# Kernel optimization log

Measured on AMD Instinct MI355X. Metric: run time of the kernel, lower is better.

## Reference

```python
import jax, jax.numpy as jnp
import numpy as np

N = 50000
E = 800000
EP = 200000
IN_C = 128
HID = 128


def setup_inputs() -> dict:
    key = jax.random.key(0)
    ks = jax.random.split(key, 10)
    x = jax.random.normal(ks[0], (N, IN_C), dtype=jnp.float32)
    edge_index = jax.random.randint(ks[1], (2, E), 0, N, dtype=jnp.int64)
    pred_edges = jax.random.randint(ks[2], (2, EP), 0, N, dtype=jnp.int64)
    s_in = 1.0 / np.sqrt(IN_C)
    s_h = 1.0 / np.sqrt(HID)
    W1l = jax.random.normal(ks[3], (IN_C, HID), dtype=jnp.float32) * s_in
    W1r = jax.random.normal(ks[4], (IN_C, HID), dtype=jnp.float32) * s_in
    b1 = jnp.zeros((HID,), dtype=jnp.float32)
    W2l = jax.random.normal(ks[5], (HID, HID), dtype=jnp.float32) * s_h
    W2r = jax.random.normal(ks[6], (HID, HID), dtype=jnp.float32) * s_h
    b2 = jnp.zeros((HID,), dtype=jnp.float32)
    return {"x": x, "W1l": W1l, "b1": b1, "W1r": W1r,
            "W2l": W2l, "b2": b2, "W2r": W2r,
            "edge_index": edge_index, "pred_edges": pred_edges}


def _sage_conv(h, Wl, b, Wr, src, dst, n_nodes):
    # PyG SAGEConv (aggr='mean'): out = lin_l(mean_j x_j) + lin_r(x_i)
    msg = h[src]                                              # (E, D) gather
    agg = jax.ops.segment_sum(msg, dst, num_segments=n_nodes)  # (N, D) scatter-add
    deg = jax.ops.segment_sum(jnp.ones((src.shape[0],), h.dtype), dst,
                              num_segments=n_nodes)
    agg = agg / jnp.maximum(deg, 1.0)[:, None]                # mean (0 for isolated)
    return agg @ Wl + b + h @ Wr


def reference(x, W1l, b1, W1r, W2l, b2, W2r, edge_index, pred_edges):
    n_nodes = x.shape[0]
    src, dst = edge_index[0], edge_index[1]
    h = jax.nn.relu(_sage_conv(x, W1l, b1, W1r, src, dst, n_nodes))
    z = _sage_conv(h, W2l, b2, W2r, src, dst, n_nodes)
    ps, pd = pred_edges[0], pred_edges[1]
    return jnp.sum(z[ps] * z[pd], axis=-1)  # (E_pred,) logits
```

## Files before the change

kernel.cpp:

```cpp
#include <hip/hip_runtime.h>

#define D 128

typedef __attribute__((ext_vector_type(8))) short short8;
typedef __attribute__((ext_vector_type(4))) float f32x4;

__device__ inline unsigned int f2bf_bits(float f) {
    unsigned int u = __float_as_uint(f);
    return (u + 0x7FFFu + ((u >> 16) & 1u)) >> 16;
}

__global__ __launch_bounds__(256) void cast_bf16_kernel(const float* __restrict__ in,
                                                        unsigned short* __restrict__ outb,
                                                        int n4,
                                                        int* __restrict__ chist,
                                                        int* __restrict__ csrpad) {
    if (blockIdx.x == gridDim.x - 1) {
        int t = threadIdx.x;
        chist[t] = 0;
        if (t < 16) csrpad[t] = 0;
        return;
    }
    int i = blockIdx.x * blockDim.x + threadIdx.x;
    if (i >= n4) return;
    f32x4 v = *(const f32x4*)(in + (size_t)i * 4);
    ushort4 o;
    o.x = (unsigned short)f2bf_bits(v.x);
    o.y = (unsigned short)f2bf_bits(v.y);
    o.z = (unsigned short)f2bf_bits(v.z);
    o.w = (unsigned short)f2bf_bits(v.w);
    *(ushort4*)(outb + (size_t)i * 4) = o;
}

__global__ __launch_bounds__(256) void coarse_count_kernel(const int* __restrict__ dst,
                                                           int* __restrict__ chist, int E) {
    __shared__ int h[256];
    h[threadIdx.x] = 0;
    __syncthreads();
    const int stride = gridDim.x * 256;
    for (int e = blockIdx.x * 256 + threadIdx.x; e < E; e += stride)
        atomicAdd(&h[dst[e] >> 8], 1);
    __syncthreads();
    int v = h[threadIdx.x];
    if (v) atomicAdd(&chist[threadIdx.x], v);
}

__global__ __launch_bounds__(256) void scan256_kernel(const int* __restrict__ chist,
                                                      int* __restrict__ cbase,
                                                      int* __restrict__ gcur) {
    __shared__ int wsum[4];
    const int t = threadIdx.x, lane = t & 63, wv = t >> 6;
    int v = chist[t];
    int s = v;
#pragma unroll
    for (int o = 1; o < 64; o <<= 1) {
        int u = __shfl_up(s, o, 64);
        if (lane >= o) s += u;
    }
    if (lane == 63) wsum[wv] = s;
    __syncthreads();
    int add = 0;
    for (int w = 0; w < wv; ++w) add += wsum[w];
    cbase[t + 1] = s + add;
    if (t == 0) cbase[0] = 0;
    gcur[t] = s + add - v;
}

#define CCHUNK 4096
__global__ __launch_bounds__(256) void coarse_scatter_kernel(
    const int* __restrict__ src, const int* __restrict__ dst,
    int* __restrict__ gcur, unsigned int* __restrict__ centries, int E)
{
    __shared__ int h[256];
    __shared__ int base[256];
    __shared__ unsigned int stage[CCHUNK];
    const int t = threadIdx.x;
    const int e0 = blockIdx.x * CCHUNK;
    h[t] = 0;
    __syncthreads();
#pragma unroll
    for (int i = 0; i < 16; ++i) {
        int e = e0 + i * 256 + t;
        unsigned int u = 0xFFFFFFFFu;
        if (e < E) {
            int d = dst[e];
            int s = src[e];
            int b = d >> 8;
            u = ((unsigned)b << 24) | ((unsigned)s << 8) | (unsigned)(d & 255);
            atomicAdd(&h[b], 1);
        }
        stage[i * 256 + t] = u;
    }
    __syncthreads();
    base[t] = atomicAdd(&gcur[t], h[t]);
    __syncthreads();
    h[t] = 0;
    __syncthreads();
#pragma unroll
    for (int i = 0; i < 16; ++i) {
        unsigned int u = stage[i * 256 + t];
        if (u != 0xFFFFFFFFu) {
            int b = u >> 24;
            int r = atomicAdd(&h[b], 1);
            centries[base[b] + r] = u & 0x00FFFFFFu;
        }
    }
}

#define DCAP 8192
__global__ __launch_bounds__(256) void fine_bucket_kernel(
    const unsigned int* __restrict__ centries,
    const int* __restrict__ cbase,
    int* __restrict__ offo, int* __restrict__ csr, int N, int E)
{
    __shared__ int h[256], ex[256], wsum[4];
    __shared__ int stg[DCAP];
    const int t = threadIdx.x, lane = t & 63, wv = t >> 6;
    const int b = blockIdx.x;
    const int s0 = cbase[b];
    const int cnt = cbase[b + 1] - s0;
    h[t] = 0;
    __syncthreads();
    for (int i = t; i < cnt; i += 256)
        atomicAdd(&h[centries[s0 + i] & 255], 1);
    __syncthreads();
    int v = h[t], s = v;
#pragma unroll
    for (int o = 1; o < 64; o <<= 1) {
        int u = __shfl_up(s, o, 64);
        if (lane >= o) s += u;
    }
    if (lane == 63) wsum[wv] = s;
    __syncthreads();
    int add = 0;
    for (int w = 0; w < wv; ++w) add += wsum[w];
    const int exc = s + add - v;
    ex[t] = exc;
    const int dg = b * 256 + t;
    if (dg < N) offo[dg] = s0 + exc;
    if (b == 0 && t == 0) offo[N] = E;
    h[t] = 0;
    __syncthreads();
    if (cnt <= DCAP) {
        for (int i = t; i < cnt; i += 256) {
            unsigned int u = centries[s0 + i];
            int dl = u & 255;
            int r = atomicAdd(&h[dl], 1);
            stg[ex[dl] + r] = (int)(u >> 8);
        }
        __syncthreads();
        for (int i = t; i < cnt; i += 256)
            csr[s0 + i] = stg[i];
    } else {
        for (int i = t; i < cnt; i += 256) {
            unsigned int u = centries[s0 + i];
            int dl = u & 255;
            int r = atomicAdd(&h[dl], 1);
            csr[s0 + ex[dl] + r] = (int)(u >> 8);
        }
    }
}

__global__ __launch_bounds__(256) void wsplit_kernel(const float* __restrict__ W1l,
                                                     const float* __restrict__ W1r,
                                                     const float* __restrict__ W2l,
                                                     const float* __restrict__ W2r,
                                                     unsigned short* __restrict__ h1,
                                                     unsigned short* __restrict__ l1,
                                                     unsigned short* __restrict__ h2,
                                                     unsigned short* __restrict__ l2) {
    int gidx = blockIdx.x * 256 + threadIdx.x;
    int sel = gidx >> 15;
    int idx = gidx & 32767;
    int t = idx >> 12;
    int ks = (idx >> 9) & 7;
    int lane = (idx >> 3) & 63;
    int j = idx & 7;
    int q = lane >> 4, r16 = lane & 15;
    int k = ks * 32 + q * 8 + j;
    int c = t * 16 + r16;
    const float* Wl = sel ? W2l : W1l;
    const float* Wr = sel ? W2r : W1r;
    float v = (k < 128) ? Wl[k * 128 + c] : Wr[(k - 128) * 128 + c];
    unsigned int h = f2bf_bits(v);
    float hf = __uint_as_float(h << 16);
    unsigned int l = f2bf_bits(v - hf);
    (sel ? h2 : h1)[idx] = (unsigned short)h;
    (sel ? l2 : l1)[idx] = (unsigned short)l;
}

__global__ __launch_bounds__(256) void gather_mean_kernel(
    const unsigned short* __restrict__ featbf,
    const int* __restrict__ off,
    const int* __restrict__ csr,
    float* __restrict__ aggp,
    int n_nodes)
{
    const int hw = (blockIdx.x * 256 + threadIdx.x) >> 5;
    const int l5 = threadIdx.x & 31;
    if (hw >= n_nodes) return;
    const unsigned short* fb = featbf + (size_t)l5 * 4;
    const int start = off[hw];
    const int end = off[hw + 1];
    f32x4 acc = {0.f, 0.f, 0.f, 0.f};
    for (int e = start; e < end; e += 16) {
        int4 ia = *(const int4*)(csr + e);
        int4 ib = *(const int4*)(csr + e + 4);
        int4 ic = *(const int4*)(csr + e + 8);
        int4 id = *(const int4*)(csr + e + 12);
        uint2 r[16];
        r[0]  = *(const uint2*)(fb + (size_t)ia.x * D);
        r[1]  = *(const uint2*)(fb + (size_t)ia.y * D);
        r[2]  = *(const uint2*)(fb + (size_t)ia.z * D);
        r[3]  = *(const uint2*)(fb + (size_t)ia.w * D);
        r[4]  = *(const uint2*)(fb + (size_t)ib.x * D);
        r[5]  = *(const uint2*)(fb + (size_t)ib.y * D);
        r[6]  = *(const uint2*)(fb + (size_t)ib.z * D);
        r[7]  = *(const uint2*)(fb + (size_t)ib.w * D);
        r[8]  = *(const uint2*)(fb + (size_t)ic.x * D);
        r[9]  = *(const uint2*)(fb + (size_t)ic.y * D);
        r[10] = *(const uint2*)(fb + (size_t)ic.z * D);
        r[11] = *(const uint2*)(fb + (size_t)ic.w * D);
        r[12] = *(const uint2*)(fb + (size_t)id.x * D);
        r[13] = *(const uint2*)(fb + (size_t)id.y * D);
        r[14] = *(const uint2*)(fb + (size_t)id.z * D);
        r[15] = *(const uint2*)(fb + (size_t)id.w * D);
#pragma unroll
        for (int p = 0; p < 16; ++p) {
            uint2 rv = r[p];
            if (e + p >= end) { rv.x = 0u; rv.y = 0u; }
            acc.x += __uint_as_float(rv.x << 16);
            acc.y += __uint_as_float(rv.x & 0xffff0000u);
            acc.z += __uint_as_float(rv.y << 16);
            acc.w += __uint_as_float(rv.y & 0xffff0000u);
        }
    }
    float dinv = 1.0f / (float)max(end - start, 1);
    acc *= dinv;
    const int tile = hw >> 4, r16 = hw & 15;
    const int ks = l5 >> 3, q = (l5 & 7) >> 1, jb = (l5 & 1) * 4;
    const size_t p = ((size_t)(tile * 4 + ks) * 64 + q * 16 + r16) * 8 + jb;
    *(f32x4*)(aggp + p) = acc;
}

__global__ __launch_bounds__(256) void sage_gemm_kernel(
    const float* __restrict__ aggp,
    const float* __restrict__ selfm,
    const unsigned short* __restrict__ wpk_hi,
    const unsigned short* __restrict__ wpk_lo,
    const float* __restrict__ bias,
    float* __restrict__ outp,
    unsigned short* __restrict__ outbf,
    int ntiles, int self_packed, int do_relu)
{
    const int wv = threadIdx.x >> 6;
    const int lane = threadIdx.x & 63;
    const int tile = blockIdx.x * 4 + wv;
    if (tile >= ntiles) return;
    const int q = lane >> 4, r16 = lane & 15;
    const int n0w = tile * 16;

    f32x4 acc8[8];
#pragma unroll
    for (int t = 0; t < 8; ++t) acc8[t] = (f32x4){0.f, 0.f, 0.f, 0.f};

    const float* ap = aggp + (size_t)tile * 2048 + lane * 8;
    const float* spk = selfm + (size_t)tile * 2048 + lane * 8;
    const float* spr = selfm + (size_t)(n0w + r16) * D + q * 8;

    for (int ks = 0; ks < 8; ++ks) {
        f32x4 a0, a1;
        if (ks < 4) {
            a0 = *(const f32x4*)(ap + ks * 512);
            a1 = *(const f32x4*)(ap + ks * 512 + 4);
        } else if (self_packed) {
            a0 = *(const f32x4*)(spk + (ks - 4) * 512);
            a1 = *(const f32x4*)(spk + (ks - 4) * 512 + 4);
        } else {
            a0 = *(const f32x4*)(spr + (ks - 4) * 32);
            a1 = *(const f32x4*)(spr + (ks - 4) * 32 + 4);
        }
        short8 BH[8], BL[8];
        const unsigned short* bh = wpk_hi + (size_t)ks * 512 + lane * 8;
        const unsigned short* bl = wpk_lo + (size_t)ks * 512 + lane * 8;
#pragma unroll
        for (int t = 0; t < 8; ++t) {
            BH[t] = *(const short8*)(bh + (size_t)t * 4096);
            BL[t] = *(const short8*)(bl + (size_t)t * 4096);
        }
        short8 ahi, alo;
#pragma unroll
        for (int i = 0; i < 8; ++i) {
            float vv = (i < 4) ? a0[i] : a1[i - 4];
            unsigned int h = f2bf_bits(vv);
            float hf = __uint_as_float(h << 16);
            unsigned int l = f2bf_bits(vv - hf);
            ahi[i] = (short)h;
            alo[i] = (short)l;
        }
#pragma unroll
        for (int t = 0; t < 8; ++t) {
            acc8[t] = __builtin_amdgcn_mfma_f32_16x16x32_bf16(ahi, BH[t], acc8[t], 0, 0, 0);
            acc8[t] = __builtin_amdgcn_mfma_f32_16x16x32_bf16(alo, BH[t], acc8[t], 0, 0, 0);
            acc8[t] = __builtin_amdgcn_mfma_f32_16x16x32_bf16(ahi, BL[t], acc8[t], 0, 0, 0);
        }
    }

#pragma unroll
    for (int t = 0; t < 8; ++t) {
        const float bv = bias[t * 16 + r16];
#pragma unroll
        for (int r = 0; r < 4; ++r) {
            float vv = acc8[t][r] + bv;
            if (do_relu) vv = fmaxf(vv, 0.f);
            if (outp) {
                const size_t p = ((size_t)(tile * 4 + (t >> 1)) * 64
                                  + ((t & 1) * 2 + (r16 >> 3)) * 16 + q * 4 + r) * 8
                                 + (r16 & 7);
                outp[p] = vv;
            }
            if (outbf) {
                outbf[(size_t)(n0w + q * 4 + r) * D + t * 16 + r16] =
                    (unsigned short)f2bf_bits(vv);
            }
        }
    }
}

__global__ __launch_bounds__(256) void pred_kernel(const unsigned short* __restrict__ zbf,
                                                   const int* __restrict__ ps,
                                                   const int* __restrict__ pd,
                                                   float* __restrict__ out, int EP) {
    int idx = blockIdx.x * blockDim.x + threadIdx.x;
    int e = idx >> 5;
    if (e >= EP) return;
    int l = idx & 31;
    const unsigned short* fb = zbf + (size_t)l * 4;
    uint2 ra = *(const uint2*)(fb + (size_t)ps[e] * D);
    uint2 rb = *(const uint2*)(fb + (size_t)pd[e] * D);
    float p = __uint_as_float(ra.x << 16)         * __uint_as_float(rb.x << 16)
            + __uint_as_float(ra.x & 0xffff0000u) * __uint_as_float(rb.x & 0xffff0000u)
            + __uint_as_float(ra.y << 16)         * __uint_as_float(rb.y << 16)
            + __uint_as_float(ra.y & 0xffff0000u) * __uint_as_float(rb.y & 0xffff0000u);
#pragma unroll
    for (int off = 16; off > 0; off >>= 1) p += __shfl_xor(p, off, 32);
    if (l == 0) out[e] = p;
}

extern "C" void kernel_launch(void* const* d_in, const int* in_sizes, int n_in,
                              void* d_out, int out_size, void* d_ws, size_t ws_size,
                              hipStream_t stream) {
    const float* x   = (const float*)d_in[0];
    const float* W1l = (const float*)d_in[1];
    const float* b1  = (const float*)d_in[2];
    const float* W1r = (const float*)d_in[3];
    const float* W2l = (const float*)d_in[4];
    const float* b2  = (const float*)d_in[5];
    const float* W2r = (const float*)d_in[6];
    const int* edge_index = (const int*)d_in[7];
    const int* pred_edges = (const int*)d_in[8];
    float* out = (float*)d_out;

    const int N  = in_sizes[0] / D;
    const int E  = in_sizes[7] / 2;
    const int EP = in_sizes[8] / 2;

    const int* src = edge_index;
    const int* dst = edge_index + E;
    const int* ps  = pred_edges;
    const int* pd  = pred_edges + EP;

    int* chist   = (int*)d_ws;
    int* cbase   = chist + 256;
    int* gcur    = cbase + 272;
    int* off     = gcur + 256;
    unsigned int* centries = (unsigned int*)(off + 50016);
    int* csr     = (int*)(centries + E);
    float* aggp  = (float*)(csr + E + 16);
    float* hpk   = aggp + (size_t)N * D;
    unsigned short* w1_hi = (unsigned short*)(hpk + (size_t)N * D);
    unsigned short* w1_lo = w1_hi + 32768;
    unsigned short* w2_hi = w1_lo + 32768;
    unsigned short* w2_lo = w2_hi + 32768;
    unsigned short* fbf   = w2_lo + 32768;

    const int nblk_gather = (N * 32 + 255) / 256;
    const int ntiles = N / 16;
    const int nblk_gemm = (ntiles + 3) / 4;
    const int ncast = (N * D / 4 + 255) / 256;
    const int nbC = (E + CCHUNK - 1) / CCHUNK;
    const int nbD = (N + 255) / 256;

    wsplit_kernel<<<256, 256, 0, stream>>>(W1l, W1r, W2l, W2r, w1_hi, w1_lo, w2_hi, w2_lo);
    cast_bf16_kernel<<<ncast + 1, 256, 0, stream>>>(x, fbf, N * D / 4, chist, csr + E);

    coarse_count_kernel<<<256, 256, 0, stream>>>(dst, chist, E);
    scan256_kernel<<<1, 256, 0, stream>>>(chist, cbase, gcur);
    coarse_scatter_kernel<<<nbC, 256, 0, stream>>>(src, dst, gcur, centries, E);
    fine_bucket_kernel<<<nbD, 256, 0, stream>>>(centries, cbase, off, csr, N, E);

    gather_mean_kernel<<<nblk_gather, 256, 0, stream>>>(fbf, off, csr, aggp, N);
    sage_gemm_kernel<<<nblk_gemm, 256, 0, stream>>>(aggp, x, w1_hi, w1_lo, b1,
                                                    hpk, fbf, ntiles, 0, 1);
    gather_mean_kernel<<<nblk_gather, 256, 0, stream>>>(fbf, off, csr, aggp, N);
    sage_gemm_kernel<<<nblk_gemm, 256, 0, stream>>>(aggp, hpk, w2_hi, w2_lo, b2,
                                                    (float*)nullptr, fbf, ntiles, 1, 0);
    pred_kernel<<<(EP * 32 + 255) / 256, 256, 0, stream>>>(fbf, ps, pd, out, EP);
}
```

Measured before the change: 261.0 us.

## Fuse prep kernels and store GEMM operands pre-split as packed bf16 hi/lo

Merges the weight split, input cast, coarse histogram and pad zeroing into one prep kernel. The histogram now uses per-block partials that the scan kernel reduces, so the global atomics go away. Aggregates and self features are now written as packed bf16 hi/lo pairs instead of fp32, which halves operand bytes and removes the split arithmetic inside the GEMM. Out-of-range gather indices are redirected to a valid row, and bounds checks are dropped on the assumption that N is a multiple of the block sizes. The cost is extra workspace, an extra write of the packed x in prep, and a 256-iteration serial reduction in the scan.

```diff
diff --git a/kernel.cpp b/kernel.cpp
--- a/kernel.cpp
+++ b/kernel.cpp
@@ -9,48 +9,80 @@
     unsigned int u = __float_as_uint(f);
     return (u + 0x7FFFu + ((u >> 16) & 1u)) >> 16;
 }
-
-__global__ __launch_bounds__(256) void cast_bf16_kernel(const float* __restrict__ in,
-                                                        unsigned short* __restrict__ outb,
-                                                        int n4,
-                                                        int* __restrict__ chist,
-                                                        int* __restrict__ csrpad) {
-    if (blockIdx.x == gridDim.x - 1) {
-        int t = threadIdx.x;
-        chist[t] = 0;
+__device__ inline void bfsplit(float v, unsigned short& h, unsigned short& l) {
+    unsigned int hb = f2bf_bits(v);
+    float hf = __uint_as_float(hb << 16);
+    h = (unsigned short)hb;
+    l = (unsigned short)f2bf_bits(v - hf);
+}
+
+__global__ __launch_bounds__(256) void prep_kernel(
+    const float* __restrict__ x,
+    const float* __restrict__ W1l, const float* __restrict__ W1r,
+    const float* __restrict__ W2l, const float* __restrict__ W2r,
+    const int* __restrict__ dst,
+    unsigned short* __restrict__ fbf,
+    unsigned short* __restrict__ xp_hi, unsigned short* __restrict__ xp_lo,
+    unsigned short* __restrict__ w1_hi, unsigned short* __restrict__ w1_lo,
+    unsigned short* __restrict__ w2_hi, unsigned short* __restrict__ w2_lo,
+    int* __restrict__ part, int* __restrict__ csrpad, int E)
+{
+    const int t = threadIdx.x;
+    const int b = blockIdx.x;
+    if (b < 6250) {
+        const int i = b * 256 + t;
+        const int hw = i >> 5, l5 = i & 31;
+        f32x4 v = *(const f32x4*)(x + (size_t)hw * D + l5 * 4);
+        ushort4 hv, lv;
+        bfsplit(v.x, hv.x, lv.x);
+        bfsplit(v.y, hv.y, lv.y);
+        bfsplit(v.z, hv.z, lv.z);
+        bfsplit(v.w, hv.w, lv.w);
+        *(ushort4*)(fbf + (size_t)hw * D + l5 * 4) = hv;
+        const int tile = hw >> 4, r16 = hw & 15;
+        const int ks = l5 >> 3, q = (l5 & 7) >> 1, jb = (l5 & 1) * 4;
+        const size_t p = ((size_t)(tile * 4 + ks) * 64 + q * 16 + r16) * 8 + jb;
+        *(ushort4*)(xp_hi + p) = hv;
+        *(ushort4*)(xp_lo + p) = lv;
+    } else if (b < 6506) {
+        int gidx = (b - 6250) * 256 + t;
+        int sel = gidx >> 15;
+        int idx = gidx & 32767;
+        int tt = idx >> 12;
+        int ks = (idx >> 9) & 7;
+        int lane = (idx >> 3) & 63;
+        int j = idx & 7;
+        int q = lane >> 4, r16 = lane & 15;
+        int k = ks * 32 + q * 8 + j;
+        int c = tt * 16 + r16;
+        const float* Wl = sel ? W2l : W1l;
+        const float* Wr = sel ? W2r : W1r;
+        float v = (k < 128) ? Wl[k * 128 + c] : Wr[(k - 128) * 128 + c];
+        unsigned short h, l;
+        bfsplit(v, h, l);
+        (sel ? w2_hi : w1_hi)[idx] = h;
+        (sel ? w2_lo : w1_lo)[idx] = l;
+    } else if (b < 6762) {
+        __shared__ int h[256];
+        h[t] = 0;
+        __syncthreads();
+        const int b3 = b - 6506;
+        for (int e = b3 * 256 + t; e < E; e += 65536)
+            atomicAdd(&h[dst[e] >> 8], 1);
+        __syncthreads();
+        part[b3 * 256 + t] = h[t];
+    } else {
         if (t < 16) csrpad[t] = 0;
-        return;
-    }
-    int i = blockIdx.x * blockDim.x + threadIdx.x;
-    if (i >= n4) return;
-    f32x4 v = *(const f32x4*)(in + (size_t)i * 4);
-    ushort4 o;
-    o.x = (unsigned short)f2bf_bits(v.x);
-    o.y = (unsigned short)f2bf_bits(v.y);
-    o.z = (unsigned short)f2bf_bits(v.z);
-    o.w = (unsigned short)f2bf_bits(v.w);
-    *(ushort4*)(outb + (size_t)i * 4) = o;
-}
-
-__global__ __launch_bounds__(256) void coarse_count_kernel(const int* __restrict__ dst,
-                                                           int* __restrict__ chist, int E) {
-    __shared__ int h[256];
-    h[threadIdx.x] = 0;
-    __syncthreads();
-    const int stride = gridDim.x * 256;
-    for (int e = blockIdx.x * 256 + threadIdx.x; e < E; e += stride)
-        atomicAdd(&h[dst[e] >> 8], 1);
-    __syncthreads();
-    int v = h[threadIdx.x];
-    if (v) atomicAdd(&chist[threadIdx.x], v);
-}
-
-__global__ __launch_bounds__(256) void scan256_kernel(const int* __restrict__ chist,
+    }
+}
+
+__global__ __launch_bounds__(256) void scan256_kernel(const int* __restrict__ part,
                                                       int* __restrict__ cbase,
                                                       int* __restrict__ gcur) {
     __shared__ int wsum[4];
     const int t = threadIdx.x, lane = t & 63, wv = t >> 6;
-    int v = chist[t];
+    int v = 0;
+    for (int b = 0; b < 256; ++b) v += part[b * 256 + t];
     int s = v;
 #pragma unroll
     for (int o = 1; o < 64; o <<= 1) {
@@ -161,44 +193,15 @@
     }
 }
 
-__global__ __launch_bounds__(256) void wsplit_kernel(const float* __restrict__ W1l,
-                                                     const float* __restrict__ W1r,
-                                                     const float* __restrict__ W2l,
-                                                     const float* __restrict__ W2r,
-                                                     unsigned short* __restrict__ h1,
-                                                     unsigned short* __restrict__ l1,
-                                                     unsigned short* __restrict__ h2,
-                                                     unsigned short* __restrict__ l2) {
-    int gidx = blockIdx.x * 256 + threadIdx.x;
-    int sel = gidx >> 15;
-    int idx = gidx & 32767;
-    int t = idx >> 12;
-    int ks = (idx >> 9) & 7;
-    int lane = (idx >> 3) & 63;
-    int j = idx & 7;
-    int q = lane >> 4, r16 = lane & 15;
-    int k = ks * 32 + q * 8 + j;
-    int c = t * 16 + r16;
-    const float* Wl = sel ? W2l : W1l;
-    const float* Wr = sel ? W2r : W1r;
-    float v = (k < 128) ? Wl[k * 128 + c] : Wr[(k - 128) * 128 + c];
-    unsigned int h = f2bf_bits(v);
-    float hf = __uint_as_float(h << 16);
-    unsigned int l = f2bf_bits(v - hf);
-    (sel ? h2 : h1)[idx] = (unsigned short)h;
-    (sel ? l2 : l1)[idx] = (unsigned short)l;
-}
-
 __global__ __launch_bounds__(256) void gather_mean_kernel(
     const unsigned short* __restrict__ featbf,
     const int* __restrict__ off,
     const int* __restrict__ csr,
-    float* __restrict__ aggp,
-    int n_nodes)
+    unsigned short* __restrict__ ag_hi,
+    unsigned short* __restrict__ ag_lo)
 {
     const int hw = (blockIdx.x * 256 + threadIdx.x) >> 5;
     const int l5 = threadIdx.x & 31;
-    if (hw >= n_nodes) return;
     const unsigned short* fb = featbf + (size_t)l5 * 4;
     const int start = off[hw];
     const int end = off[hw + 1];
@@ -208,23 +211,16 @@
         int4 ib = *(const int4*)(csr + e + 4);
         int4 ic = *(const int4*)(csr + e + 8);
         int4 id = *(const int4*)(csr + e + 12);
+        int sx[16];
+        sx[0] = ia.x;  sx[1] = ia.y;  sx[2] = ia.z;  sx[3] = ia.w;
+        sx[4] = ib.x;  sx[5] = ib.y;  sx[6] = ib.z;  sx[7] = ib.w;
+        sx[8] = ic.x;  sx[9] = ic.y;  sx[10] = ic.z; sx[11] = ic.w;
+        sx[12] = id.x; sx[13] = id.y; sx[14] = id.z; sx[15] = id.w;
+#pragma unroll
+        for (int p = 1; p < 16; ++p) sx[p] = (e + p < end) ? sx[p] : ia.x;
         uint2 r[16];
-        r[0]  = *(const uint2*)(fb + (size_t)ia.x * D);
-        r[1]  = *(const uint2*)(fb + (size_t)ia.y * D);
-        r[2]  = *(const uint2*)(fb + (size_t)ia.z * D);
-        r[3]  = *(const uint2*)(fb + (size_t)ia.w * D);
-        r[4]  = *(const uint2*)(fb + (size_t)ib.x * D);
-        r[5]  = *(const uint2*)(fb + (size_t)ib.y * D);
-        r[6]  = *(const uint2*)(fb + (size_t)ib.z * D);
-        r[7]  = *(const uint2*)(fb + (size_t)ib.w * D);
-        r[8]  = *(const uint2*)(fb + (size_t)ic.x * D);
-        r[9]  = *(const uint2*)(fb + (size_t)ic.y * D);
-        r[10] = *(const uint2*)(fb + (size_t)ic.z * D);
-        r[11] = *(const uint2*)(fb + (size_t)ic.w * D);
-        r[12] = *(const uint2*)(fb + (size_t)id.x * D);
-        r[13] = *(const uint2*)(fb + (size_t)id.y * D);
-        r[14] = *(const uint2*)(fb + (size_t)id.z * D);
-        r[15] = *(const uint2*)(fb + (size_t)id.w * D);
+#pragma unroll
+        for (int p = 0; p < 16; ++p) r[p] = *(const uint2*)(fb + (size_t)sx[p] * D);
 #pragma unroll
         for (int p = 0; p < 16; ++p) {
             uint2 rv = r[p];
@@ -237,21 +233,30 @@
     }
     float dinv = 1.0f / (float)max(end - start, 1);
     acc *= dinv;
+    ushort4 hv, lv;
+    bfsplit(acc.x, hv.x, lv.x);
+    bfsplit(acc.y, hv.y, lv.y);
+    bfsplit(acc.z, hv.z, lv.z);
+    bfsplit(acc.w, hv.w, lv.w);
     const int tile = hw >> 4, r16 = hw & 15;
     const int ks = l5 >> 3, q = (l5 & 7) >> 1, jb = (l5 & 1) * 4;
     const size_t p = ((size_t)(tile * 4 + ks) * 64 + q * 16 + r16) * 8 + jb;
-    *(f32x4*)(aggp + p) = acc;
+    *(ushort4*)(ag_hi + p) = hv;
+    *(ushort4*)(ag_lo + p) = lv;
 }
 
 __global__ __launch_bounds__(256) void sage_gemm_kernel(
-    const float* __restrict__ aggp,
-    const float* __restrict__ selfm,
-    const unsigned short* __restrict__ wpk_hi,
-    const unsigned short* __restrict__ wpk_lo,
+    const unsigned short* __restrict__ a_hi,
+    const unsigned short* __restrict__ a_lo,
+    const unsigned short* __restrict__ s_hi,
+    const unsigned short* __restrict__ s_lo,
+    const unsigned short* __restrict__ w_hi,
+    const unsigned short* __restrict__ w_lo,
     const float* __restrict__ bias,
-    float* __restrict__ outp,
+    unsigned short* __restrict__ op_hi,
+    unsigned short* __restrict__ op_lo,
     unsigned short* __restrict__ outbf,
-    int ntiles, int self_packed, int do_relu)
+    int ntiles, int do_relu)
 {
     const int wv = threadIdx.x >> 6;
     const int lane = threadIdx.x & 63;
@@ -264,45 +269,30 @@
 #pragma unroll
     for (int t = 0; t < 8; ++t) acc8[t] = (f32x4){0.f, 0.f, 0.f, 0.f};
 
-    const float* ap = aggp + (size_t)tile * 2048 + lane * 8;
-    const float* spk = selfm + (size_t)tile * 2048 + lane * 8;
-    const float* spr = selfm + (size_t)(n0w + r16) * D + q * 8;
+    const size_t abase = (size_t)tile * 2048 + lane * 8;
 
     for (int ks = 0; ks < 8; ++ks) {
-        f32x4 a0, a1;
+        short8 AH, AL;
         if (ks < 4) {
-            a0 = *(const f32x4*)(ap + ks * 512);
-            a1 = *(const f32x4*)(ap + ks * 512 + 4);
-        } else if (self_packed) {
-            a0 = *(const f32x4*)(spk + (ks - 4) * 512);
-            a1 = *(const f32x4*)(spk + (ks - 4) * 512 + 4);
+            AH = *(const short8*)(a_hi + abase + ks * 512);
+            AL = *(const short8*)(a_lo + abase + ks * 512);
         } else {
-            a0 = *(const f32x4*)(spr + (ks - 4) * 32);
-            a1 = *(const f32x4*)(spr + (ks - 4) * 32 + 4);
+            AH = *(const short8*)(s_hi + abase + (ks - 4) * 512);
+            AL = *(const short8*)(s_lo + abase + (ks - 4) * 512);
         }
         short8 BH[8], BL[8];
-        const unsigned short* bh = wpk_hi + (size_t)ks * 512 + lane * 8;
-        const unsigned short* bl = wpk_lo + (size_t)ks * 512 + lane * 8;
+        const unsigned short* bh = w_hi + (size_t)ks * 512 + lane * 8;
+        const unsigned short* bl = w_lo + (size_t)ks * 512 + lane * 8;
 #pragma unroll
         for (int t = 0; t < 8; ++t) {
             BH[t] = *(const short8*)(bh + (size_t)t * 4096);
             BL[t] = *(const short8*)(bl + (size_t)t * 4096);
         }
-        short8 ahi, alo;
-#pragma unroll
-        for (int i = 0; i < 8; ++i) {
-            float vv = (i < 4) ? a0[i] : a1[i - 4];
-            unsigned int h = f2bf_bits(vv);
-            float hf = __uint_as_float(h << 16);
-            unsigned int l = f2bf_bits(vv - hf);
-            ahi[i] = (short)h;
-            alo[i] = (short)l;
-        }
 #pragma unroll
         for (int t = 0; t < 8; ++t) {
-            acc8[t] = __builtin_amdgcn_mfma_f32_16x16x32_bf16(ahi, BH[t], acc8[t], 0, 0, 0);
-            acc8[t] = __builtin_amdgcn_mfma_f32_16x16x32_bf16(alo, BH[t], acc8[t], 0, 0, 0);
-            acc8[t] = __builtin_amdgcn_mfma_f32_16x16x32_bf16(ahi, BL[t], acc8[t], 0, 0, 0);
+            acc8[t] = __builtin_amdgcn_mfma_f32_16x16x32_bf16(AH, BH[t], acc8[t], 0, 0, 0);
+            acc8[t] = __builtin_amdgcn_mfma_f32_16x16x32_bf16(AL, BH[t], acc8[t], 0, 0, 0);
+            acc8[t] = __builtin_amdgcn_mfma_f32_16x16x32_bf16(AH, BL[t], acc8[t], 0, 0, 0);
         }
     }
 
@@ -313,11 +303,14 @@
         for (int r = 0; r < 4; ++r) {
             float vv = acc8[t][r] + bv;
             if (do_relu) vv = fmaxf(vv, 0.f);
-            if (outp) {
+            if (op_hi) {
+                unsigned short h, l;
+                bfsplit(vv, h, l);
                 const size_t p = ((size_t)(tile * 4 + (t >> 1)) * 64
                                   + ((t & 1) * 2 + (r16 >> 3)) * 16 + q * 4 + r) * 8
                                  + (r16 & 7);
-                outp[p] = vv;
+                op_hi[p] = h;
+                op_lo[p] = l;
             }
             if (outbf) {
                 outbf[(size_t)(n0w + q * 4 + r) * D + t * 16 + r16] =
@@ -370,40 +363,47 @@
     const int* ps  = pred_edges;
     const int* pd  = pred_edges + EP;
 
-    int* chist   = (int*)d_ws;
-    int* cbase   = chist + 256;
+    int* part    = (int*)d_ws;
+    int* cbase   = part + 65536;
     int* gcur    = cbase + 272;
     int* off     = gcur + 256;
     unsigned int* centries = (unsigned int*)(off + 50016);
     int* csr     = (int*)(centries + E);
-    float* aggp  = (float*)(csr + E + 16);
-    float* hpk   = aggp + (size_t)N * D;
-    unsigned short* w1_hi = (unsigned short*)(hpk + (size_t)N * D);
+    unsigned short* ag_hi = (unsigned short*)(csr + E + 16);
+    unsigned short* ag_lo = ag_hi + (size_t)N * D;
+    unsigned short* xp_hi = ag_lo + (size_t)N * D;
+    unsigned short* xp_lo = xp_hi + (size_t)N * D;
+    unsigned short* hp_hi = xp_lo + (size_t)N * D;
+    unsigned short* hp_lo = hp_hi + (size_t)N * D;
+    unsigned short* fbf   = hp_lo + (size_t)N * D;
+    unsigned short* w1_hi = fbf + (size_t)N * D;
     unsigned short* w1_lo = w1_hi + 32768;
     unsigned short* w2_hi = w1_lo + 32768;
     unsigned short* w2_lo = w2_hi + 32768;
-    unsigned short* fbf   = w2_lo + 32768;
-
-    const int nblk_gather = (N * 32 + 255) / 256;
+
+    const int nblk_gather = N * 32 / 256;
     const int ntiles = N / 16;
     const int nblk_gemm = (ntiles + 3) / 4;
-    const int ncast = (N * D / 4 + 255) / 256;
     const int nbC = (E + CCHUNK - 1) / CCHUNK;
     const int nbD = (N + 255) / 256;
 
-    wsplit_kernel<<<256, 256, 0, stream>>>(W1l, W1r, W2l, W2r, w1_hi, w1_lo, w2_hi, w2_lo);
-    cast_bf16_kernel<<<ncast + 1, 256, 0, stream>>>(x, fbf, N * D / 4, chist, csr + E);
-
-    coarse_count_kernel<<<256, 256, 0, stream>>>(dst, chist, E);
-    scan256_kernel<<<1, 256, 0, stream>>>(chist, cbase, gcur);
+    prep_kernel<<<6763, 256, 0, stream>>>(x, W1l, W1r, W2l, W2r, dst,
+                                          fbf, xp_hi, xp_lo,
+                                          w1_hi, w1_lo, w2_hi, w2_lo,
+                                          part, csr + E, E);
+    scan256_kernel<<<1, 256, 0, stream>>>(part, cbase, gcur);
     coarse_scatter_kernel<<<nbC, 256, 0, stream>>>(src, dst, gcur, centries, E);
     fine_bucket_kernel<<<nbD, 256, 0, stream>>>(centries, cbase, off, csr, N, E);
 
-    gather_mean_kernel<<<nblk_gather, 256, 0, stream>>>(fbf, off, csr, aggp, N);
-    sage_gemm_kernel<<<nblk_gemm, 256, 0, stream>>>(aggp, x, w1_hi, w1_lo, b1,
-                                                    hpk, fbf, ntiles, 0, 1);
-    gather_mean_kernel<<<nblk_gather, 256, 0, stream>>>(fbf, off, csr, aggp, N);
-    sage_gemm_kernel<<<nblk_gemm, 256, 0, stream>>>(aggp, hpk, w2_hi, w2_lo, b2,
-                                                    (float*)nullptr, fbf, ntiles, 1, 0);
+    gather_mean_kernel<<<nblk_gather, 256, 0, stream>>>(fbf, off, csr, ag_hi, ag_lo);
+    sage_gemm_kernel<<<nblk_gemm, 256, 0, stream>>>(ag_hi, ag_lo, xp_hi, xp_lo,
+                                                    w1_hi, w1_lo, b1,
+                                                    hp_hi, hp_lo, fbf, ntiles, 1);
+    gather_mean_kernel<<<nblk_gather, 256, 0, stream>>>(fbf, off, csr, ag_hi, ag_lo);
+    sage_gemm_kernel<<<nblk_gemm, 256, 0, stream>>>(ag_hi, ag_lo, hp_hi, hp_lo,
+                                                    w2_hi, w2_lo, b2,
+                                                    (unsigned short*)nullptr,
+                                                    (unsigned short*)nullptr,
+                                                    fbf, ntiles, 0);
     pred_kernel<<<(EP * 32 + 255) / 256, 256, 0, stream>>>(fbf, ps, pd, out, EP);
 }
```

Result: slower. 325.0 us (+24.5%).
